# Optimization experiments

Measured on AMD Instinct MI355X. Metric: run time of the kernel, lower is better.

The kernel has to match this reference:

```python
import jax, jax.numpy as jnp
import numpy as np

N_NODES = 500_000
N_EDGES = 5_000_000
D = 16


def setup_inputs() -> dict:
    key = jax.random.key(0)
    k1, k2, k3, k4 = jax.random.split(key, 4)
    x = jax.random.normal(k1, (N_NODES, D), dtype=jnp.float32)
    edge_index = jax.random.randint(k2, (2, N_EDGES), 0, N_NODES, dtype=jnp.int32)
    # SAGEConv params: lin_l (applied to aggregated neighbors, carries bias),
    # lin_r (applied to root/self features, no bias). Torch Linear stores W as [out, in].
    scale = 1.0 / np.sqrt(D)
    W_l = jax.random.uniform(k3, (D, D), minval=-scale, maxval=scale, dtype=jnp.float32)
    b_l = jnp.zeros((D,), dtype=jnp.float32)
    W_r = jax.random.uniform(k4, (D, D), minval=-scale, maxval=scale, dtype=jnp.float32)
    return {"x": x, "edge_index": edge_index, "W_l": W_l, "b_l": b_l, "W_r": W_r}


def reference(x, edge_index, W_l, b_l, W_r):
    src = edge_index[0]  # message sources (x_j)
    dst = edge_index[1]  # aggregation targets (i)
    n = x.shape[0]
    # mean aggregation of neighbor features per destination node
    agg = jax.ops.segment_sum(x[src], dst, num_segments=n)  # [N, D]
    cnt = jax.ops.segment_sum(jnp.ones((src.shape[0],), dtype=x.dtype), dst, num_segments=n)
    mean = agg / jnp.maximum(cnt, 1.0)[:, None]
    # out = lin_l(mean) + lin_r(x)
    return mean @ W_l.T + b_l + x @ W_r.T
```

## Files before the change

kernel.cpp:

```cpp
#include <hip/hip_runtime.h>

#define N_NODES 500000
#define N_EDGES 5000000
#define D 16
#define BSH 9
#define BSZ 512
#define NB ((N_NODES + BSZ - 1) / BSZ)
#define CH 16384
#define PBLK ((N_EDGES + CH - 1) / CH)

__global__ __launch_bounds__(256) void hist_k(const int* __restrict__ edst,
                                              int* __restrict__ bhist) {
    __shared__ int h[NB];
    for (int i = threadIdx.x; i < NB; i += 256) h[i] = 0;
    __syncthreads();
    int stride = gridDim.x * blockDim.x;
    for (int e = blockIdx.x * blockDim.x + threadIdx.x; e < N_EDGES; e += stride)
        atomicAdd(&h[edst[e] >> BSH], 1);
    __syncthreads();
    for (int i = threadIdx.x; i < NB; i += 256)
        if (h[i]) atomicAdd(&bhist[i], h[i]);
}

__global__ void scan_k(const int* __restrict__ bhist, int* __restrict__ boff,
                       int* __restrict__ cursor) {
    __shared__ int s[1024];
    int t = threadIdx.x;
    int v = (t < NB) ? bhist[t] : 0;
    s[t] = v; __syncthreads();
    for (int off = 1; off < 1024; off <<= 1) {
        int u = (t >= off) ? s[t - off] : 0;
        __syncthreads(); s[t] += u; __syncthreads();
    }
    if (t < NB) { int ex = s[t] - v; boff[t] = ex; cursor[t] = ex; }
    if (t == 0) boff[NB] = N_EDGES;
}

__global__ __launch_bounds__(256) void place_k(const int* __restrict__ esrc,
                                               const int* __restrict__ edst,
                                               int* __restrict__ cursor,
                                               unsigned* __restrict__ rec) {
    __shared__ int lc[NB];
    int t = threadIdx.x;
    for (int i = t; i < NB; i += 256) lc[i] = 0;
    __syncthreads();
    int e0 = blockIdx.x * CH;
    int e1 = e0 + CH; if (e1 > N_EDGES) e1 = N_EDGES;
    for (int e = e0 + t; e < e1; e += 256)
        atomicAdd(&lc[edst[e] >> BSH], 1);
    __syncthreads();
    for (int i = t; i < NB; i += 256) {
        int c = lc[i];
        if (c) lc[i] = atomicAdd(&cursor[i], c);
    }
    __syncthreads();
    for (int e = e0 + t; e < e1; e += 256) {
        int dd = edst[e];
        int b = dd >> BSH;
        int p = atomicAdd(&lc[b], 1);
        rec[p] = ((unsigned)(dd & (BSZ - 1)) << 19) | (unsigned)esrc[e];
    }
}

__global__ __launch_bounds__(512, 8) void reduce_k(
    const float* __restrict__ x, const unsigned* __restrict__ rec,
    const int* __restrict__ boff, const float* __restrict__ Wl,
    const float* __restrict__ bl, const float* __restrict__ Wr,
    float* __restrict__ out) {
    __shared__ float slice[BSZ * D];
    __shared__ int scnt[BSZ];
    __shared__ unsigned srec[1024];
    int t = threadIdx.x;
    for (int i = t; i < BSZ * D; i += 512) slice[i] = 0.f;
    for (int i = t; i < BSZ; i += 512) scnt[i] = 0;

    int d = t & 15, g = t >> 4;
    int b = blockIdx.x;
    int beg = boff[b], end = boff[b + 1];

    for (int c0 = beg; c0 < end; c0 += 1024) {
        int cn = end - c0; if (cn > 1024) cn = 1024;
        __syncthreads();
        for (int i = t; i < cn; i += 512) srec[i] = rec[c0 + i];
        __syncthreads();
#pragma unroll 4
        for (int i = g; i < cn; i += 32) {
            unsigned rc = srec[i];
            int src = (int)(rc & 0x7FFFFu);
            int nl  = (int)(rc >> 19);
            float v = x[src * D + d];
            atomicAdd(&slice[nl * D + d], v);
            if (d == 0) atomicAdd(&scnt[nl], 1);
        }
    }
    __syncthreads();

    float wl[D], wr[D];
    const float4* wl4 = (const float4*)(Wl + d * D);
    const float4* wr4 = (const float4*)(Wr + d * D);
#pragma unroll
    for (int q = 0; q < 4; ++q) {
        float4 a = wl4[q], b2 = wr4[q];
        wl[4*q]=a.x; wl[4*q+1]=a.y; wl[4*q+2]=a.z; wl[4*q+3]=a.w;
        wr[4*q]=b2.x; wr[4*q+1]=b2.y; wr[4*q+2]=b2.z; wr[4*q+3]=b2.w;
    }
    float bb = bl[d];
    int node0 = b << BSH;
    for (int n = g; n < BSZ; n += 32) {
        int node = node0 + n;
        if (node >= N_NODES) break;
        float m  = slice[n * D + d] / fmaxf((float)scnt[n], 1.f);
        float xv = x[node * D + d];
        float o  = bb;
#pragma unroll
        for (int k = 0; k < D; ++k)
            o += __shfl(m, k, 16) * wl[k] + __shfl(xv, k, 16) * wr[k];
        out[node * D + d] = o;
    }
}

__global__ void sage_scatter(const float* __restrict__ x, const int* __restrict__ esrc,
                             const int* __restrict__ edst, float* __restrict__ agg,
                             float* __restrict__ cnt) {
    long long gid = (long long)blockIdx.x * blockDim.x + threadIdx.x;
    long long e = gid >> 4;
    int d = (int)(gid & 15);
    if (e >= N_EDGES) return;
    atomicAdd(&agg[(long long)edst[e] * D + d], x[(long long)esrc[e] * D + d]);
    if (d == 0) atomicAdd(&cnt[edst[e]], 1.0f);
}

__global__ void sage_finalize(const float* __restrict__ x, float* __restrict__ agg_out,
                              const float* __restrict__ cnt, const float* __restrict__ W_l,
                              const float* __restrict__ b_l, const float* __restrict__ W_r) {
    __shared__ float sWl[D * D], sWr[D * D], sb[D];
    int tid = threadIdx.x;
    if (tid < D * D) { sWl[tid] = W_l[tid]; sWr[tid] = W_r[tid]; }
    if (tid < D) sb[tid] = b_l[tid];
    __syncthreads();
    int i = blockIdx.x * blockDim.x + tid;
    if (i >= N_NODES) return;
    float inv = 1.0f / fmaxf(cnt[i], 1.0f);
    float m[D], xv[D];
    const float4* ap = (const float4*)(agg_out + (long long)i * D);
    const float4* xp = (const float4*)(x + (long long)i * D);
#pragma unroll
    for (int q = 0; q < 4; ++q) {
        float4 a = ap[q], b = xp[q];
        m[4*q]=a.x*inv; m[4*q+1]=a.y*inv; m[4*q+2]=a.z*inv; m[4*q+3]=a.w*inv;
        xv[4*q]=b.x; xv[4*q+1]=b.y; xv[4*q+2]=b.z; xv[4*q+3]=b.w;
    }
    float o[D];
#pragma unroll
    for (int oo = 0; oo < D; ++oo) {
        float a2 = sb[oo];
#pragma unroll
        for (int k = 0; k < D; ++k) a2 += m[k]*sWl[oo*D+k] + xv[k]*sWr[oo*D+k];
        o[oo] = a2;
    }
    float4* op = (float4*)(agg_out + (long long)i * D);
#pragma unroll
    for (int q = 0; q < 4; ++q)
        op[q] = make_float4(o[4*q], o[4*q+1], o[4*q+2], o[4*q+3]);
}

extern "C" void kernel_launch(void* const* d_in, const int* in_sizes, int n_in,
                              void* d_out, int out_size, void* d_ws, size_t ws_size,
                              hipStream_t stream) {
    const float* x   = (const float*)d_in[0];
    const int*   ei  = (const int*)d_in[1];
    const float* W_l = (const float*)d_in[2];
    const float* b_l = (const float*)d_in[3];
    const float* W_r = (const float*)d_in[4];
    const int* esrc = ei;
    const int* edst = ei + N_EDGES;
    float* out = (float*)d_out;

    size_t rec_b = (size_t)N_EDGES * 4;
    size_t need  = rec_b + (size_t)(3 * NB + 1) * 4;

    if (ws_size >= need) {
        unsigned* rec = (unsigned*)d_ws;
        int* bhist  = (int*)((char*)d_ws + rec_b);
        int* boff   = bhist + NB;
        int* cursor = boff + (NB + 1);

        hipMemsetAsync(bhist, 0, (size_t)NB * 4, stream);
        hist_k<<<512, 256, 0, stream>>>(edst, bhist);
        scan_k<<<1, 1024, 0, stream>>>(bhist, boff, cursor);
        place_k<<<PBLK, 256, 0, stream>>>(esrc, edst, cursor, rec);
        reduce_k<<<NB, 512, 0, stream>>>(x, rec, boff, W_l, b_l, W_r, out);
    } else {
        float* cntf = (float*)d_ws;
        hipMemsetAsync(out, 0, (size_t)N_NODES * D * sizeof(float), stream);
        hipMemsetAsync(cntf, 0, (size_t)N_NODES * sizeof(float), stream);
        long long total = (long long)N_EDGES * D;
        sage_scatter<<<(unsigned)((total + 255) / 256), 256, 0, stream>>>(x, esrc, edst, out, cntf);
        sage_finalize<<<(N_NODES + 255) / 256, 256, 0, stream>>>(x, out, cntf, W_l, b_l, W_r);
    }
}
```

Measured before the change: 595.0 us.

## Gather fp16 feature chunks in column-split passes and move linear layers to separate kernel

```diff
diff --git a/kernel.cpp b/kernel.cpp
--- a/kernel.cpp
+++ b/kernel.cpp
@@ -1,4 +1,5 @@
 #include <hip/hip_runtime.h>
+#include <hip/hip_fp16.h>
 
 #define N_NODES 500000
 #define N_EDGES 5000000
@@ -8,6 +9,25 @@
 #define NB ((N_NODES + BSZ - 1) / BSZ)
 #define CH 16384
 #define PBLK ((N_EDGES + CH - 1) / CH)
+#define NCK 4
+#define SLP 5
+
+__global__ __launch_bounds__(256) void conv_k(const float* __restrict__ x,
+                                              uint2* __restrict__ xh) {
+    int i = blockIdx.x * blockDim.x + threadIdx.x;
+    if (i >= N_NODES) return;
+    const float4* xr = (const float4*)(x + (size_t)i * D);
+#pragma unroll
+    for (int c = 0; c < NCK; ++c) {
+        float4 v = xr[c];
+        __half2 a = __floats2half2_rn(v.x, v.y);
+        __half2 b = __floats2half2_rn(v.z, v.w);
+        uint2 u;
+        u.x = *reinterpret_cast<unsigned*>(&a);
+        u.y = *reinterpret_cast<unsigned*>(&b);
+        xh[(size_t)c * N_NODES + i] = u;
+    }
+}
 
 __global__ __launch_bounds__(256) void hist_k(const int* __restrict__ edst,
                                               int* __restrict__ bhist) {
@@ -56,67 +76,93 @@
     __syncthreads();
     for (int e = e0 + t; e < e1; e += 256) {
         int dd = edst[e];
-        int b = dd >> BSH;
-        int p = atomicAdd(&lc[b], 1);
+        int p = atomicAdd(&lc[dd >> BSH], 1);
         rec[p] = ((unsigned)(dd & (BSZ - 1)) << 19) | (unsigned)esrc[e];
     }
 }
 
 __global__ __launch_bounds__(512, 8) void reduce_k(
-    const float* __restrict__ x, const unsigned* __restrict__ rec,
-    const int* __restrict__ boff, const float* __restrict__ Wl,
-    const float* __restrict__ bl, const float* __restrict__ Wr,
-    float* __restrict__ out) {
-    __shared__ float slice[BSZ * D];
+    const uint2* __restrict__ xh, const unsigned* __restrict__ rec,
+    const int* __restrict__ boff, float* __restrict__ sum,
+    int* __restrict__ cnt) {
+    __shared__ float slice[BSZ * SLP];
     __shared__ int scnt[BSZ];
-    __shared__ unsigned srec[1024];
     int t = threadIdx.x;
-    for (int i = t; i < BSZ * D; i += 512) slice[i] = 0.f;
-    for (int i = t; i < BSZ; i += 512) scnt[i] = 0;
-
-    int d = t & 15, g = t >> 4;
     int b = blockIdx.x;
     int beg = boff[b], end = boff[b + 1];
-
-    for (int c0 = beg; c0 < end; c0 += 1024) {
-        int cn = end - c0; if (cn > 1024) cn = 1024;
+    int node0 = b << BSH;
+
+#pragma unroll 1
+    for (int c = 0; c < NCK; ++c) {
+        for (int i = t; i < BSZ * SLP; i += 512) slice[i] = 0.f;
+        if (c == 0) scnt[t] = 0;
         __syncthreads();
-        for (int i = t; i < cn; i += 512) srec[i] = rec[c0 + i];
+
+        const uint2* tab = xh + (size_t)c * N_NODES;
+        for (int i = beg + t; i < end; i += 512) {
+            unsigned rc = __builtin_nontemporal_load(&rec[i]);
+            int nl = (int)(rc >> 19);
+            int s  = (int)(rc & 0x7FFFFu);
+            uint2 u = tab[s];
+            __half2 h0 = *reinterpret_cast<__half2*>(&u.x);
+            __half2 h1 = *reinterpret_cast<__half2*>(&u.y);
+            float2 f0 = __half22float2(h0);
+            float2 f1 = __half22float2(h1);
+            int base = nl * SLP;
+            atomicAdd(&slice[base + 0], f0.x);
+            atomicAdd(&slice[base + 1], f0.y);
+            atomicAdd(&slice[base + 2], f1.x);
+            atomicAdd(&slice[base + 3], f1.y);
+            if (c == 0) atomicAdd(&scnt[nl], 1);
+        }
         __syncthreads();
-#pragma unroll 4
-        for (int i = g; i < cn; i += 32) {
-            unsigned rc = srec[i];
-            int src = (int)(rc & 0x7FFFFu);
-            int nl  = (int)(rc >> 19);
-            float v = x[src * D + d];
-            atomicAdd(&slice[nl * D + d], v);
-            if (d == 0) atomicAdd(&scnt[nl], 1);
+
+        int node = node0 + t;
+        if (node < N_NODES) {
+            float4 s4 = make_float4(slice[t * SLP], slice[t * SLP + 1],
+                                    slice[t * SLP + 2], slice[t * SLP + 3]);
+            ((float4*)sum)[(size_t)node * NCK + c] = s4;
+            if (c == 0) cnt[node] = scnt[t];
         }
-    }
-    __syncthreads();
-
-    float wl[D], wr[D];
-    const float4* wl4 = (const float4*)(Wl + d * D);
-    const float4* wr4 = (const float4*)(Wr + d * D);
+        __syncthreads();
+    }
+}
+
+__global__ __launch_bounds__(256) void final_k(const float* __restrict__ x,
+                                               float* __restrict__ sum_out,
+                                               const int* __restrict__ cnt,
+                                               const float* __restrict__ Wl,
+                                               const float* __restrict__ bl,
+                                               const float* __restrict__ Wr) {
+    __shared__ float sWl[D * D], sWr[D * D], sb[D];
+    int tid = threadIdx.x;
+    if (tid < D * D) { sWl[tid] = Wl[tid]; sWr[tid] = Wr[tid]; }
+    if (tid < D) sb[tid] = bl[tid];
+    __syncthreads();
+    int i = blockIdx.x * blockDim.x + tid;
+    if (i >= N_NODES) return;
+    float inv = 1.0f / fmaxf((float)cnt[i], 1.0f);
+    float m[D], xv[D];
+    const float4* ap = (const float4*)(sum_out + (size_t)i * D);
+    const float4* xp = (const float4*)(x + (size_t)i * D);
 #pragma unroll
     for (int q = 0; q < 4; ++q) {
-        float4 a = wl4[q], b2 = wr4[q];
-        wl[4*q]=a.x; wl[4*q+1]=a.y; wl[4*q+2]=a.z; wl[4*q+3]=a.w;
-        wr[4*q]=b2.x; wr[4*q+1]=b2.y; wr[4*q+2]=b2.z; wr[4*q+3]=b2.w;
-    }
-    float bb = bl[d];
-    int node0 = b << BSH;
-    for (int n = g; n < BSZ; n += 32) {
-        int node = node0 + n;
-        if (node >= N_NODES) break;
-        float m  = slice[n * D + d] / fmaxf((float)scnt[n], 1.f);
-        float xv = x[node * D + d];
-        float o  = bb;
-#pragma unroll
-        for (int k = 0; k < D; ++k)
-            o += __shfl(m, k, 16) * wl[k] + __shfl(xv, k, 16) * wr[k];
-        out[node * D + d] = o;
-    }
+        float4 a = ap[q], b = xp[q];
+        m[4*q]=a.x*inv; m[4*q+1]=a.y*inv; m[4*q+2]=a.z*inv; m[4*q+3]=a.w*inv;
+        xv[4*q]=b.x; xv[4*q+1]=b.y; xv[4*q+2]=b.z; xv[4*q+3]=b.w;
+    }
+    float o[D];
+#pragma unroll
+    for (int oo = 0; oo < D; ++oo) {
+        float a2 = sb[oo];
+#pragma unroll
+        for (int k = 0; k < D; ++k) a2 += m[k]*sWl[oo*D+k] + xv[k]*sWr[oo*D+k];
+        o[oo] = a2;
+    }
+    float4* op = (float4*)(sum_out + (size_t)i * D);
+#pragma unroll
+    for (int q = 0; q < 4; ++q)
+        op[q] = make_float4(o[4*q], o[4*q+1], o[4*q+2], o[4*q+3]);
 }
 
 __global__ void sage_scatter(const float* __restrict__ x, const int* __restrict__ esrc,
@@ -176,20 +222,26 @@
     const int* edst = ei + N_EDGES;
     float* out = (float*)d_out;
 
-    size_t rec_b = (size_t)N_EDGES * 4;
-    size_t need  = rec_b + (size_t)(3 * NB + 1) * 4;
+    size_t xh_b   = (size_t)NCK * N_NODES * 8;
+    size_t rec_b  = (size_t)N_EDGES * 4;
+    size_t cnt_b  = (size_t)N_NODES * 4;
+    size_t need   = xh_b + rec_b + cnt_b + (size_t)(3 * NB + 1) * 4;
 
     if (ws_size >= need) {
-        unsigned* rec = (unsigned*)d_ws;
-        int* bhist  = (int*)((char*)d_ws + rec_b);
-        int* boff   = bhist + NB;
-        int* cursor = boff + (NB + 1);
+        uint2*    xh     = (uint2*)d_ws;
+        unsigned* rec    = (unsigned*)((char*)d_ws + xh_b);
+        int*      cnt    = (int*)((char*)d_ws + xh_b + rec_b);
+        int*      bhist  = cnt + N_NODES;
+        int*      boff   = bhist + NB;
+        int*      cursor = boff + (NB + 1);
 
         hipMemsetAsync(bhist, 0, (size_t)NB * 4, stream);
+        conv_k<<<(N_NODES + 255) / 256, 256, 0, stream>>>(x, xh);
         hist_k<<<512, 256, 0, stream>>>(edst, bhist);
         scan_k<<<1, 1024, 0, stream>>>(bhist, boff, cursor);
         place_k<<<PBLK, 256, 0, stream>>>(esrc, edst, cursor, rec);
-        reduce_k<<<NB, 512, 0, stream>>>(x, rec, boff, W_l, b_l, W_r, out);
+        reduce_k<<<NB, 512, 0, stream>>>(xh, rec, boff, out, cnt);
+        final_k<<<(N_NODES + 255) / 256, 256, 0, stream>>>(x, out, cnt, W_l, b_l, W_r);
     } else {
         float* cntf = (float*)d_ws;
         hipMemsetAsync(out, 0, (size_t)N_NODES * D * sizeof(float), stream);
```

New measurement: 583.6 us. Within noise of the previous version (-1.9%).

## Gather from fp16 channel-major copy of x in bucketed reduce

Applied to the files above, without the earlier changes.

```diff
diff --git a/kernel.cpp b/kernel.cpp
--- a/kernel.cpp
+++ b/kernel.cpp
@@ -1,4 +1,5 @@
 #include <hip/hip_runtime.h>
+#include <hip/hip_fp16.h>
 
 #define N_NODES 500000
 #define N_EDGES 5000000
@@ -8,6 +9,22 @@
 #define NB ((N_NODES + BSZ - 1) / BSZ)
 #define CH 16384
 #define PBLK ((N_EDGES + CH - 1) / CH)
+#define NCK 8
+#define SLP 17
+#define SRCAP 5632
+
+__global__ __launch_bounds__(256) void conv_k(const float* __restrict__ x,
+                                              unsigned* __restrict__ xt) {
+    int i = blockIdx.x * blockDim.x + threadIdx.x;
+    if (i >= N_NODES) return;
+    const float2* xr = (const float2*)(x + (size_t)i * D);
+#pragma unroll
+    for (int c = 0; c < NCK; ++c) {
+        float2 v = xr[c];
+        __half2 h = __floats2half2_rn(v.x, v.y);
+        xt[(size_t)c * N_NODES + i] = *reinterpret_cast<unsigned*>(&h);
+    }
+}
 
 __global__ __launch_bounds__(256) void hist_k(const int* __restrict__ edst,
                                               int* __restrict__ bhist) {
@@ -56,45 +73,65 @@
     __syncthreads();
     for (int e = e0 + t; e < e1; e += 256) {
         int dd = edst[e];
-        int b = dd >> BSH;
-        int p = atomicAdd(&lc[b], 1);
+        int p = atomicAdd(&lc[dd >> BSH], 1);
         rec[p] = ((unsigned)(dd & (BSZ - 1)) << 19) | (unsigned)esrc[e];
     }
 }
 
-__global__ __launch_bounds__(512, 8) void reduce_k(
-    const float* __restrict__ x, const unsigned* __restrict__ rec,
-    const int* __restrict__ boff, const float* __restrict__ Wl,
-    const float* __restrict__ bl, const float* __restrict__ Wr,
-    float* __restrict__ out) {
-    __shared__ float slice[BSZ * D];
+__global__ __launch_bounds__(512, 2) void reduce_k(
+    const float* __restrict__ x, const unsigned* __restrict__ xt,
+    const unsigned* __restrict__ rec, const int* __restrict__ boff,
+    const float* __restrict__ Wl, const float* __restrict__ bl,
+    const float* __restrict__ Wr, float* __restrict__ out) {
+    __shared__ float slice[BSZ * SLP];
+    __shared__ unsigned srec[SRCAP];
     __shared__ int scnt[BSZ];
-    __shared__ unsigned srec[1024];
     int t = threadIdx.x;
-    for (int i = t; i < BSZ * D; i += 512) slice[i] = 0.f;
-    for (int i = t; i < BSZ; i += 512) scnt[i] = 0;
-
-    int d = t & 15, g = t >> 4;
+    for (int i = t; i < BSZ * SLP; i += 512) slice[i] = 0.f;
+    scnt[t] = 0;
+    __syncthreads();
+
     int b = blockIdx.x;
     int beg = boff[b], end = boff[b + 1];
-
-    for (int c0 = beg; c0 < end; c0 += 1024) {
-        int cn = end - c0; if (cn > 1024) cn = 1024;
+    int n = end - beg;
+    int ns = n < SRCAP ? n : SRCAP;
+
+    for (int i = t; i < ns; i += 512) {
+        unsigned rc = __builtin_nontemporal_load(&rec[beg + i]);
+        srec[i] = rc;
+        atomicAdd(&scnt[rc >> 19], 1);
+    }
+    for (int i = SRCAP + t; i < n; i += 512) {
+        unsigned rc = __builtin_nontemporal_load(&rec[beg + i]);
+        atomicAdd(&scnt[rc >> 19], 1);
+    }
+    __syncthreads();
+
+#pragma unroll 1
+    for (int c = 0; c < NCK; ++c) {
+        const unsigned* tab = xt + (size_t)c * N_NODES;
+        for (int i = t; i < ns; i += 512) {
+            unsigned rc = srec[i];
+            unsigned u = tab[rc & 0x7FFFFu];
+            __half2 h = *reinterpret_cast<__half2*>(&u);
+            float2 f = __half22float2(h);
+            int base = (int)(rc >> 19) * SLP + 2 * c;
+            atomicAdd(&slice[base], f.x);
+            atomicAdd(&slice[base + 1], f.y);
+        }
+        for (int i = SRCAP + t; i < n; i += 512) {
+            unsigned rc = __builtin_nontemporal_load(&rec[beg + i]);
+            unsigned u = tab[rc & 0x7FFFFu];
+            __half2 h = *reinterpret_cast<__half2*>(&u);
+            float2 f = __half22float2(h);
+            int base = (int)(rc >> 19) * SLP + 2 * c;
+            atomicAdd(&slice[base], f.x);
+            atomicAdd(&slice[base + 1], f.y);
+        }
         __syncthreads();
-        for (int i = t; i < cn; i += 512) srec[i] = rec[c0 + i];
-        __syncthreads();
-#pragma unroll 4
-        for (int i = g; i < cn; i += 32) {
-            unsigned rc = srec[i];
-            int src = (int)(rc & 0x7FFFFu);
-            int nl  = (int)(rc >> 19);
-            float v = x[src * D + d];
-            atomicAdd(&slice[nl * D + d], v);
-            if (d == 0) atomicAdd(&scnt[nl], 1);
-        }
-    }
-    __syncthreads();
-
+    }
+
+    int d = t & 15, g = t >> 4;
     float wl[D], wr[D];
     const float4* wl4 = (const float4*)(Wl + d * D);
     const float4* wr4 = (const float4*)(Wr + d * D);
@@ -106,10 +143,10 @@
     }
     float bb = bl[d];
     int node0 = b << BSH;
-    for (int n = g; n < BSZ; n += 32) {
-        int node = node0 + n;
+    for (int nn = g; nn < BSZ; nn += 32) {
+        int node = node0 + nn;
         if (node >= N_NODES) break;
-        float m  = slice[n * D + d] / fmaxf((float)scnt[n], 1.f);
+        float m  = slice[nn * SLP + d] / fmaxf((float)scnt[nn], 1.f);
         float xv = x[node * D + d];
         float o  = bb;
 #pragma unroll
@@ -176,20 +213,23 @@
     const int* edst = ei + N_EDGES;
     float* out = (float*)d_out;
 
+    size_t xt_b  = (size_t)NCK * N_NODES * 4;
     size_t rec_b = (size_t)N_EDGES * 4;
-    size_t need  = rec_b + (size_t)(3 * NB + 1) * 4;
+    size_t need  = xt_b + rec_b + (size_t)(3 * NB + 1) * 4;
 
     if (ws_size >= need) {
-        unsigned* rec = (unsigned*)d_ws;
-        int* bhist  = (int*)((char*)d_ws + rec_b);
-        int* boff   = bhist + NB;
-        int* cursor = boff + (NB + 1);
+        unsigned* xt     = (unsigned*)d_ws;
+        unsigned* rec    = (unsigned*)((char*)d_ws + xt_b);
+        int*      bhist  = (int*)((char*)d_ws + xt_b + rec_b);
+        int*      boff   = bhist + NB;
+        int*      cursor = boff + (NB + 1);
 
         hipMemsetAsync(bhist, 0, (size_t)NB * 4, stream);
+        conv_k<<<(N_NODES + 255) / 256, 256, 0, stream>>>(x, xt);
         hist_k<<<512, 256, 0, stream>>>(edst, bhist);
         scan_k<<<1, 1024, 0, stream>>>(bhist, boff, cursor);
         place_k<<<PBLK, 256, 0, stream>>>(esrc, edst, cursor, rec);
-        reduce_k<<<NB, 512, 0, stream>>>(x, rec, boff, W_l, b_l, W_r, out);
+        reduce_k<<<NB, 512, 0, stream>>>(x, xt, rec, boff, W_l, b_l, W_r, out);
     } else {
         float* cntf = (float*)d_ws;
         hipMemsetAsync(out, 0, (size_t)N_NODES * D * sizeof(float), stream);
```

Result: no change. 602.4 us (+1.2%).
